# Optimization experiments

Hardware: AMD Instinct MI355X
Metric: run time of the kernel (lower is better)

## Reference

```python
import jax, jax.numpy as jnp
import numpy as np

N, M = 120000, 32
VX, VY = 0.16, 0.16
X_OFF = VX / 2 + 0.0          # vx/2 + pc_range[0]
Y_OFF = VY / 2 + (-39.68)     # vy/2 + pc_range[1]
BN_EPS = 1e-3


def setup_inputs() -> dict:
    key = jax.random.key(0)
    k1, k2, k3, k4, k5 = jax.random.split(key, 5)
    features = jax.random.normal(k1, (N, M, 4), dtype=jnp.float32)
    num_points = jax.random.randint(k2, (N,), 1, M + 1)              # >=1 point per pillar
    cy = jax.random.randint(k3, (N, 1), 0, 496)
    cx = jax.random.randint(k4, (N, 1), 0, 432)
    zeros = jnp.zeros((N, 2), dtype=jnp.int32)
    coors = jnp.concatenate([zeros, cy, cx], axis=1)                 # (N,4): [b, z, y, x]
    W = jax.random.normal(k5, (63, 9), dtype=jnp.float32) * 0.1      # Linear(9->63), no bias
    gamma = jnp.ones((63,), jnp.float32)
    beta = jnp.zeros((63,), jnp.float32)
    running_mean = jnp.zeros((63,), jnp.float32)
    running_var = jnp.ones((63,), jnp.float32)
    return {"features": features, "num_points": num_points, "coors": coors,
            "W": W, "gamma": gamma, "beta": beta,
            "running_mean": running_mean, "running_var": running_var}


def reference(features, num_points, coors, W, gamma, beta, running_mean, running_var):
    dt = features.dtype
    npf = num_points.astype(dt)[:, None, None]                        # (N,1,1)
    # distance to pillar centroid (xyz mean over points)
    voxels_mean = features[:, :, :3].sum(axis=1, keepdims=True) / npf
    centroid_dist = features[:, :, :3] - voxels_mean                  # (N,M,3)
    # offset from pillar base center (detached in the original)
    fxy = jax.lax.stop_gradient(features[:, :, :2])
    cx = fxy[:, :, 0] - (coors[:, 3].astype(dt)[:, None] * VX + X_OFF)
    cy = fxy[:, :, 1] - (coors[:, 2].astype(dt)[:, None] * VY + Y_OFF)
    base_center = jnp.stack([cx, cy], axis=-1)                        # (N,M,2)
    feats = jnp.concatenate([features, centroid_dist, base_center], axis=-1)  # (N,M,9)
    # zero out padded points
    mask = (jnp.arange(feats.shape[1])[None, :] < num_points[:, None]).astype(dt)[:, :, None]
    feats = feats * mask
    # PFNLayer (last layer, mode='max'): linear -> BN (eval stats) -> relu -> max over points
    x = jnp.einsum('nmc,uc->nmu', feats, W)                           # (N,M,63)
    inv = gamma / jnp.sqrt(running_var + BN_EPS)
    x = x * inv + (beta - running_mean * inv)
    x = jax.nn.relu(x)
    x_max = x.max(axis=1)                                             # (N,63)
    return jnp.concatenate([x_max, num_points.astype(dt)[:, None]], axis=-1)  # (N,64)
```

## Files before the change

### kernel.cpp

```cpp
#include <hip/hip_runtime.h>
#include <hip/hip_bf16.h>

typedef unsigned int u32;
typedef __attribute__((ext_vector_type(8))) short bf16x8;
typedef __attribute__((ext_vector_type(16))) float f32x16;
typedef __attribute__((ext_vector_type(4))) u32 u32x4;


#define XOFF (0.08f)
#define YOFF (0.08f - 39.68f)

__device__ __forceinline__ u32 f2bf_bits(float f) {
    union { float f; u32 u; } v; v.f = f;
    u32 u = v.u;
    u += 0x7fffu + ((u >> 16) & 1u);
    return u >> 16;
}
__device__ __forceinline__ short bf1(float f) { return (short)f2bf_bits(f); }

__device__ __forceinline__ u32 pk2(float lo, float hi) {
    __hip_bfloat162 h = __float22bfloat162_rn(make_float2(lo, hi));
    union { __hip_bfloat162 h; u32 u; } v; v.h = h;
    return v.u;
}

__device__ __forceinline__ float vmax16(const f32x16 v) {
    float m = fmaxf(fmaxf(v[0], v[1]), v[2]);
    m = fmaxf(fmaxf(m, v[3]), v[4]);
    m = fmaxf(fmaxf(m, v[5]), v[6]);
    m = fmaxf(fmaxf(m, v[7]), v[8]);
    m = fmaxf(fmaxf(m, v[9]), v[10]);
    m = fmaxf(fmaxf(m, v[11]), v[12]);
    m = fmaxf(fmaxf(m, v[13]), v[14]);
    return fmaxf(m, v[15]);
}

__global__ __launch_bounds__(256, 4)
void pfn_mfma(const float* __restrict__ features,
              const int* __restrict__ num_points,
              const int* __restrict__ coors,
              const float* __restrict__ W,
              const float* __restrict__ gamma,
              const float* __restrict__ beta,
              const float* __restrict__ rmean,
              const float* __restrict__ rvar,
              float* __restrict__ out,
              int n_total)
{
    const int lane = threadIdx.x & 63;
    const int wid  = threadIdx.x >> 6;
    const int half = lane >> 5;
    const int m    = lane & 31;
    const int waves_total = gridDim.x * 4;
    const int gwave = blockIdx.x * 4 + wid;

    const int c0 = m, c1 = 32 + m;
    const float inv0   = gamma[c0] / sqrtf(rvar[c0] + 1e-3f);
    const float shift0 = beta[c0] - rmean[c0] * inv0;
    float inv1 = 0.0f, shift1 = 0.0f;
    if (c1 < 63) {
        inv1   = gamma[c1] / sqrtf(rvar[c1] + 1e-3f);
        shift1 = beta[c1] - rmean[c1] * inv1;
    }

    bf16x8 b0, b1;
#pragma unroll
    for (int j = 0; j < 8; ++j) {
        const int k = half * 8 + j;
        float w0v = 0.0f, w1v = 0.0f;
        if (k < 9)       { w0v = W[c0 * 9 + k] * inv0;
                           w1v = (c1 < 63) ? W[c1 * 9 + k] * inv1 : 0.0f; }
        else if (k == 9) { w0v = shift0; w1v = shift1; }
        b0[j] = bf1(w0v);
        b1[j] = bf1(w1v);
    }

    const f32x16 zacc = {};
    const float4* featv = reinterpret_cast<const float4*>(features);
    const int n_pairs = (n_total + 1) >> 1;
    const int iters = (n_pairs + waves_total - 1) / waves_total;

    int pair = gwave;
    int nh   = min(min(pair, n_pairs - 1) * 2 + half, n_total - 1);
    int npts = num_points[nh];
    int2 cc  = *reinterpret_cast<const int2*>(coors + nh * 4 + 2);
    float4 q = featv[nh * 32 + m];

    for (int it = 0; it < iters; ++it) {
        const int pn  = pair + waves_total;
        const int nhn = min(min(pn, n_pairs - 1) * 2 + half, n_total - 1);
        const int npn = num_points[nhn];
        const int2 ccn = *reinterpret_cast<const int2*>(coors + nhn * 4 + 2);
        const float4 qn = featv[nhn * 32 + m];

        float sx = q.x, sy = q.y, sz = q.z;
#pragma unroll
        for (int d = 1; d < 32; d <<= 1) {
            sx += __shfl_xor(sx, d, 32);
            sy += __shfl_xor(sy, d, 32);
            sz += __shfl_xor(sz, d, 32);
        }
        const float rnp = __builtin_amdgcn_rcpf((float)npts);
        const float mx = sx * rnp, my = sy * rnp, mz = sz * rnp;
        const float cxo = (float)cc.y * 0.16f + XOFF;
        const float cyo = (float)cc.x * 0.16f + YOFF;

        u32 p0 = pk2(q.x, q.y);
        u32 p1 = pk2(q.z, q.w);
        u32 p2 = pk2(q.x - mx, q.y - my);
        u32 p3 = pk2(q.z - mz, q.x - cxo);
        if (m >= npts) { p0 = 0; p1 = 0; p2 = 0; p3 = 0; }
        const u32 p4 = pk2((m < npts) ? q.y - cyo : 0.0f, 1.0f);

        const u32 x0 = __shfl_xor(p0, 32);
        const u32 x1 = __shfl_xor(p1, 32);
        const u32 x2 = __shfl_xor(p2, 32);
        const u32 x3 = __shfl_xor(p3, 32);
        const u32 x4 = __shfl_xor(p4, 32);

        u32x4 adw, bdw;
        adw[0] = half ? x4 : p0;  adw[1] = half ? 0u : p1;
        adw[2] = half ? 0u : p2;  adw[3] = half ? 0u : p3;
        bdw[0] = half ? p4 : x0;  bdw[1] = half ? 0u : x1;
        bdw[2] = half ? 0u : x2;  bdw[3] = half ? 0u : x3;
        const bf16x8 aA = __builtin_bit_cast(bf16x8, adw);
        const bf16x8 aB = __builtin_bit_cast(bf16x8, bdw);

        const f32x16 cA0 = __builtin_amdgcn_mfma_f32_32x32x16_bf16(aA, b0, zacc, 0, 0, 0);
        const f32x16 cA1 = __builtin_amdgcn_mfma_f32_32x32x16_bf16(aA, b1, zacc, 0, 0, 0);
        float tA0 = vmax16(cA0);
        float tA1 = vmax16(cA1);
        const f32x16 cB0 = __builtin_amdgcn_mfma_f32_32x32x16_bf16(aB, b0, zacc, 0, 0, 0);
        const f32x16 cB1 = __builtin_amdgcn_mfma_f32_32x32x16_bf16(aB, b1, zacc, 0, 0, 0);
        float tB0 = vmax16(cB0);
        float tB1 = vmax16(cB1);

        tA0 = fmaxf(tA0, __shfl_xor(tA0, 32));
        tA1 = fmaxf(tA1, __shfl_xor(tA1, 32));
        tB0 = fmaxf(tB0, __shfl_xor(tB0, 32));
        tB1 = fmaxf(tB1, __shfl_xor(tB1, 32));

        float vA = fmaxf(half ? tA1 : tA0, 0.0f);
        float vB = fmaxf(half ? tB1 : tB0, 0.0f);

        const float npf = (float)npts;
        const float npA = __shfl(npf, 0);
        const float npB = __shfl(npf, 32);
        if (lane == 63) { vA = npA; vB = npB; }

        if (pair < n_pairs) {
            const int nA = pair * 2;
            out[nA * 64 + lane] = vA;
            if (nA + 1 < n_total) out[(nA + 1) * 64 + lane] = vB;
        }

        pair = pn; q = qn; npts = npn; cc = ccn;
    }
}

extern "C" void kernel_launch(void* const* d_in, const int* in_sizes, int n_in,
                              void* d_out, int out_size, void* d_ws, size_t ws_size,
                              hipStream_t stream) {
    const float* features   = (const float*)d_in[0];
    const int*   num_points = (const int*)d_in[1];
    const int*   coors      = (const int*)d_in[2];
    const float* W          = (const float*)d_in[3];
    const float* gamma      = (const float*)d_in[4];
    const float* beta       = (const float*)d_in[5];
    const float* rmean      = (const float*)d_in[6];
    const float* rvar       = (const float*)d_in[7];
    float* out              = (float*)d_out;

    const int n_total = in_sizes[1];

    const int blocks = 2048;
    pfn_mfma<<<blocks, 256, 0, stream>>>(features, num_points, coors, W,
                                         gamma, beta, rmean, rvar, out, n_total);
}
```

Before: 125.2 us.

## Process two pillar pairs per iteration with ds_swizzle reductions and deeper prefetch

```diff
diff --git a/kernel.cpp b/kernel.cpp
--- a/kernel.cpp
+++ b/kernel.cpp
@@ -9,6 +9,10 @@
 
 #define XOFF (0.08f)
 #define YOFF (0.08f - 39.68f)
+
+#define SWZ_ADD(s, imm)                                                        \
+    s += __builtin_bit_cast(float, __builtin_amdgcn_ds_swizzle(                \
+             __builtin_bit_cast(int, s), imm))
 
 __device__ __forceinline__ u32 f2bf_bits(float f) {
     union { float f; u32 u; } v; v.f = f;
@@ -33,6 +37,77 @@
     m = fmaxf(fmaxf(m, v[11]), v[12]);
     m = fmaxf(fmaxf(m, v[13]), v[14]);
     return fmaxf(m, v[15]);
+}
+
+__device__ __forceinline__ void frontend(const float4 q, const int npts,
+                                         const int2 cc, const int m,
+                                         const int half,
+                                         bf16x8& aA, bf16x8& aB)
+{
+    float sx = q.x, sy = q.y, sz = q.z;
+    SWZ_ADD(sx, 0x041F); SWZ_ADD(sy, 0x041F); SWZ_ADD(sz, 0x041F);
+    SWZ_ADD(sx, 0x081F); SWZ_ADD(sy, 0x081F); SWZ_ADD(sz, 0x081F);
+    SWZ_ADD(sx, 0x101F); SWZ_ADD(sy, 0x101F); SWZ_ADD(sz, 0x101F);
+    SWZ_ADD(sx, 0x201F); SWZ_ADD(sy, 0x201F); SWZ_ADD(sz, 0x201F);
+    SWZ_ADD(sx, 0x401F); SWZ_ADD(sy, 0x401F); SWZ_ADD(sz, 0x401F);
+
+    const float rnp = __builtin_amdgcn_rcpf((float)npts);
+    const float mx = sx * rnp, my = sy * rnp, mz = sz * rnp;
+    const float cxo = (float)cc.y * 0.16f + XOFF;
+    const float cyo = (float)cc.x * 0.16f + YOFF;
+
+    u32 p0 = pk2(q.x, q.y);
+    u32 p1 = pk2(q.z, q.w);
+    u32 p2 = pk2(q.x - mx, q.y - my);
+    u32 p3 = pk2(q.z - mz, q.x - cxo);
+    if (m >= npts) { p0 = 0; p1 = 0; p2 = 0; p3 = 0; }
+    const u32 p4 = pk2((m < npts) ? q.y - cyo : 0.0f, 1.0f);
+
+    const u32 x0 = __shfl_xor(p0, 32);
+    const u32 x1 = __shfl_xor(p1, 32);
+    const u32 x2 = __shfl_xor(p2, 32);
+    const u32 x3 = __shfl_xor(p3, 32);
+    const u32 x4 = __shfl_xor(p4, 32);
+
+    u32x4 adw, bdw;
+    adw[0] = half ? x4 : p0;  adw[1] = half ? 0u : p1;
+    adw[2] = half ? 0u : p2;  adw[3] = half ? 0u : p3;
+    bdw[0] = half ? p4 : x0;  bdw[1] = half ? 0u : x1;
+    bdw[2] = half ? 0u : x2;  bdw[3] = half ? 0u : x3;
+    aA = __builtin_bit_cast(bf16x8, adw);
+    aB = __builtin_bit_cast(bf16x8, bdw);
+}
+
+__device__ __forceinline__ void backend(const bf16x8 aA, const bf16x8 aB,
+                                        const bf16x8 b0, const bf16x8 b1,
+                                        const f32x16 zacc, const int half,
+                                        const int lane, const float npf,
+                                        const int pairIdx, const int n_pairs,
+                                        const int n_total,
+                                        float* __restrict__ out)
+{
+    const f32x16 cA0 = __builtin_amdgcn_mfma_f32_32x32x16_bf16(aA, b0, zacc, 0, 0, 0);
+    const f32x16 cA1 = __builtin_amdgcn_mfma_f32_32x32x16_bf16(aA, b1, zacc, 0, 0, 0);
+    const float tA0 = vmax16(cA0);
+    const float tA1 = vmax16(cA1);
+    const f32x16 cB0 = __builtin_amdgcn_mfma_f32_32x32x16_bf16(aB, b0, zacc, 0, 0, 0);
+    const f32x16 cB1 = __builtin_amdgcn_mfma_f32_32x32x16_bf16(aB, b1, zacc, 0, 0, 0);
+    const float tB0 = vmax16(cB0);
+    const float tB1 = vmax16(cB1);
+
+    const float keepA = half ? tA1 : tA0, sendA = half ? tA0 : tA1;
+    const float keepB = half ? tB1 : tB0, sendB = half ? tB0 : tB1;
+    float vA = fmaxf(fmaxf(keepA, __shfl_xor(sendA, 32)), 0.0f);
+    float vB = fmaxf(fmaxf(keepB, __shfl_xor(sendB, 32)), 0.0f);
+
+    const float npo = __shfl_xor(npf, 32);
+    if (lane == 63) { vA = npo; vB = npf; }
+
+    if (pairIdx < n_pairs) {
+        const int nA = pairIdx * 2;
+        out[nA * 64 + lane] = vA;
+        if (nA + 1 < n_total) out[(nA + 1) * 64 + lane] = vB;
+    }
 }
 
 __global__ __launch_bounds__(256, 4)
@@ -78,83 +153,39 @@
     const f32x16 zacc = {};
     const float4* featv = reinterpret_cast<const float4*>(features);
     const int n_pairs = (n_total + 1) >> 1;
-    const int iters = (n_pairs + waves_total - 1) / waves_total;
-
-    int pair = gwave;
-    int nh   = min(min(pair, n_pairs - 1) * 2 + half, n_total - 1);
-    int npts = num_points[nh];
-    int2 cc  = *reinterpret_cast<const int2*>(coors + nh * 4 + 2);
-    float4 q = featv[nh * 32 + m];
+    const int stride  = waves_total * 2;
+    const int iters   = (n_pairs + stride - 1) / stride;
+
+    auto load_pair = [&](int pr, float4& q, int& np, int2& cc) {
+        int nh = min(pr, n_pairs - 1) * 2 + half;
+        nh = min(nh, n_total - 1);
+        np = num_points[nh];
+        cc = *reinterpret_cast<const int2*>(coors + nh * 4 + 2);
+        q  = featv[nh * 32 + m];
+    };
+
+    int pa = gwave;
+    float4 qa, qb; int na_, nb_; int2 ca, cb;
+    load_pair(pa, qa, na_, ca);
+    load_pair(pa + waves_total, qb, nb_, cb);
 
     for (int it = 0; it < iters; ++it) {
-        const int pn  = pair + waves_total;
-        const int nhn = min(min(pn, n_pairs - 1) * 2 + half, n_total - 1);
-        const int npn = num_points[nhn];
-        const int2 ccn = *reinterpret_cast<const int2*>(coors + nhn * 4 + 2);
-        const float4 qn = featv[nhn * 32 + m];
-
-        float sx = q.x, sy = q.y, sz = q.z;
-#pragma unroll
-        for (int d = 1; d < 32; d <<= 1) {
-            sx += __shfl_xor(sx, d, 32);
-            sy += __shfl_xor(sy, d, 32);
-            sz += __shfl_xor(sz, d, 32);
-        }
-        const float rnp = __builtin_amdgcn_rcpf((float)npts);
-        const float mx = sx * rnp, my = sy * rnp, mz = sz * rnp;
-        const float cxo = (float)cc.y * 0.16f + XOFF;
-        const float cyo = (float)cc.x * 0.16f + YOFF;
-
-        u32 p0 = pk2(q.x, q.y);
-        u32 p1 = pk2(q.z, q.w);
-        u32 p2 = pk2(q.x - mx, q.y - my);
-        u32 p3 = pk2(q.z - mz, q.x - cxo);
-        if (m >= npts) { p0 = 0; p1 = 0; p2 = 0; p3 = 0; }
-        const u32 p4 = pk2((m < npts) ? q.y - cyo : 0.0f, 1.0f);
-
-        const u32 x0 = __shfl_xor(p0, 32);
-        const u32 x1 = __shfl_xor(p1, 32);
-        const u32 x2 = __shfl_xor(p2, 32);
-        const u32 x3 = __shfl_xor(p3, 32);
-        const u32 x4 = __shfl_xor(p4, 32);
-
-        u32x4 adw, bdw;
-        adw[0] = half ? x4 : p0;  adw[1] = half ? 0u : p1;
-        adw[2] = half ? 0u : p2;  adw[3] = half ? 0u : p3;
-        bdw[0] = half ? p4 : x0;  bdw[1] = half ? 0u : x1;
-        bdw[2] = half ? 0u : x2;  bdw[3] = half ? 0u : x3;
-        const bf16x8 aA = __builtin_bit_cast(bf16x8, adw);
-        const bf16x8 aB = __builtin_bit_cast(bf16x8, bdw);
-
-        const f32x16 cA0 = __builtin_amdgcn_mfma_f32_32x32x16_bf16(aA, b0, zacc, 0, 0, 0);
-        const f32x16 cA1 = __builtin_amdgcn_mfma_f32_32x32x16_bf16(aA, b1, zacc, 0, 0, 0);
-        float tA0 = vmax16(cA0);
-        float tA1 = vmax16(cA1);
-        const f32x16 cB0 = __builtin_amdgcn_mfma_f32_32x32x16_bf16(aB, b0, zacc, 0, 0, 0);
-        const f32x16 cB1 = __builtin_amdgcn_mfma_f32_32x32x16_bf16(aB, b1, zacc, 0, 0, 0);
-        float tB0 = vmax16(cB0);
-        float tB1 = vmax16(cB1);
-
-        tA0 = fmaxf(tA0, __shfl_xor(tA0, 32));
-        tA1 = fmaxf(tA1, __shfl_xor(tA1, 32));
-        tB0 = fmaxf(tB0, __shfl_xor(tB0, 32));
-        tB1 = fmaxf(tB1, __shfl_xor(tB1, 32));
-
-        float vA = fmaxf(half ? tA1 : tA0, 0.0f);
-        float vB = fmaxf(half ? tB1 : tB0, 0.0f);
-
-        const float npf = (float)npts;
-        const float npA = __shfl(npf, 0);
-        const float npB = __shfl(npf, 32);
-        if (lane == 63) { vA = npA; vB = npB; }
-
-        if (pair < n_pairs) {
-            const int nA = pair * 2;
-            out[nA * 64 + lane] = vA;
-            if (nA + 1 < n_total) out[(nA + 1) * 64 + lane] = vB;
-        }
-
-        pair = pn; q = qn; npts = npn; cc = ccn;
+        float4 qan, qbn; int nan_, nbn_; int2 can, cbn;
+        load_pair(pa + stride, qan, nan_, can);
+        load_pair(pa + stride + waves_total, qbn, nbn_, cbn);
+
+        bf16x8 aA1, aB1, aA2, aB2;
+        frontend(qa, na_, ca, m, half, aA1, aB1);
+        frontend(qb, nb_, cb, m, half, aA2, aB2);
+
+        backend(aA1, aB1, b0, b1, zacc, half, lane, (float)na_,
+                pa,               n_pairs, n_total, out);
+        backend(aA2, aB2, b0, b1, zacc, half, lane, (float)nb_,
+                pa + waves_total, n_pairs, n_total, out);
+
+        pa += stride;
+        qa = qan; na_ = nan_; ca = can;
+        qb = qbn; nb_ = nbn_; cb = cbn;
     }
 }
 
```

New measurement: 125.0 us. About the same (-0.1%).

## Fold centroid and offset terms into the weights and compute sums with MFMA

Applied to the files above, without the earlier changes.

```diff
diff --git a/kernel.cpp b/kernel.cpp
--- a/kernel.cpp
+++ b/kernel.cpp
@@ -33,6 +33,27 @@
     m = fmaxf(fmaxf(m, v[11]), v[12]);
     m = fmaxf(fmaxf(m, v[13]), v[14]);
     return fmaxf(m, v[15]);
+}
+
+__device__ __forceinline__ float vsum16(const f32x16 v) {
+    const float a = (v[0] + v[1]) + (v[2] + v[3]);
+    const float b = (v[4] + v[5]) + (v[6] + v[7]);
+    const float c = (v[8] + v[9]) + (v[10] + v[11]);
+    const float d = (v[12] + v[13]) + (v[14] + v[15]);
+    return (a + b) + (c + d);
+}
+
+__device__ __forceinline__ float bc0(float v) {
+    return __builtin_bit_cast(float,
+        __builtin_amdgcn_ds_swizzle(__builtin_bit_cast(int, v), 0x0000));
+}
+__device__ __forceinline__ float bc1(float v) {
+    return __builtin_bit_cast(float,
+        __builtin_amdgcn_ds_swizzle(__builtin_bit_cast(int, v), 0x0020));
+}
+__device__ __forceinline__ float bc2(float v) {
+    return __builtin_bit_cast(float,
+        __builtin_amdgcn_ds_swizzle(__builtin_bit_cast(int, v), 0x0040));
 }
 
 __global__ __launch_bounds__(256, 4)
@@ -62,99 +83,132 @@
         inv1   = gamma[c1] / sqrtf(rvar[c1] + 1e-3f);
         shift1 = beta[c1] - rmean[c1] * inv1;
     }
-
-    bf16x8 b0, b1;
+    const float shift_me = half ? shift1 : shift0;
+
+    float wp0[9], wp1[9];
+#pragma unroll
+    for (int c = 0; c < 9; ++c) {
+        wp0[c] = W[c0 * 9 + c] * inv0;
+        wp1[c] = (c1 < 63) ? W[c1 * 9 + c] * inv1 : 0.0f;
+    }
+    auto rowv = [](int k, const float* wp, float sh) -> float {
+        switch (k) {
+            case 0:  return wp[0] + wp[4] + wp[7];
+            case 1:  return wp[1] + wp[5] + wp[8];
+            case 2:  return wp[2] + wp[6];
+            case 3:  return wp[3];
+            case 4:  return -30000.0f;
+            case 5:  return sh;
+            case 6:  return wp[4];
+            case 7:  return wp[5];
+            case 8:  return wp[6];
+            case 9:  return wp[7];
+            case 10: return wp[8];
+            default: return 0.0f;
+        }
+    };
+    bf16x8 b0, b1, bs;
 #pragma unroll
     for (int j = 0; j < 8; ++j) {
         const int k = half * 8 + j;
-        float w0v = 0.0f, w1v = 0.0f;
-        if (k < 9)       { w0v = W[c0 * 9 + k] * inv0;
-                           w1v = (c1 < 63) ? W[c1 * 9 + k] * inv1 : 0.0f; }
-        else if (k == 9) { w0v = shift0; w1v = shift1; }
-        b0[j] = bf1(w0v);
-        b1[j] = bf1(w1v);
+        b0[j] = bf1(rowv(k, wp0, shift0));
+        b1[j] = bf1(rowv(k, wp1, shift1));
+        bs[j] = (half == 0 && j == m && m < 3) ? bf1(1.0f) : (short)0;
     }
 
     const f32x16 zacc = {};
     const float4* featv = reinterpret_cast<const float4*>(features);
     const int n_pairs = (n_total + 1) >> 1;
-    const int iters = (n_pairs + waves_total - 1) / waves_total;
-
-    int pair = gwave;
-    int nh   = min(min(pair, n_pairs - 1) * 2 + half, n_total - 1);
-    int npts = num_points[nh];
-    int2 cc  = *reinterpret_cast<const int2*>(coors + nh * 4 + 2);
-    float4 q = featv[nh * 32 + m];
+    const int iters   = (n_pairs + waves_total - 1) / waves_total;
+
+    struct PairIn { float4 q; int npA, npB; int2 ccA, ccB; };
+    auto load_pair = [&](int pr) -> PairIn {
+        PairIn r;
+        const int base = min(pr, n_pairs - 1) * 2;
+        const int iB   = min(base + 1, n_total - 1);
+        const int nh   = min(base + half, n_total - 1);
+        r.npA = num_points[base];
+        r.npB = num_points[iB];
+        r.ccA = *reinterpret_cast<const int2*>(coors + base * 4 + 2);
+        r.ccB = *reinterpret_cast<const int2*>(coors + iB * 4 + 2);
+        r.q   = featv[nh * 32 + m];
+        return r;
+    };
+
+    int pa = gwave;
+    PairIn cur = load_pair(pa);
 
     for (int it = 0; it < iters; ++it) {
-        const int pn  = pair + waves_total;
-        const int nhn = min(min(pn, n_pairs - 1) * 2 + half, n_total - 1);
-        const int npn = num_points[nhn];
-        const int2 ccn = *reinterpret_cast<const int2*>(coors + nhn * 4 + 2);
-        const float4 qn = featv[nhn * 32 + m];
-
-        float sx = q.x, sy = q.y, sz = q.z;
-#pragma unroll
-        for (int d = 1; d < 32; d <<= 1) {
-            sx += __shfl_xor(sx, d, 32);
-            sy += __shfl_xor(sy, d, 32);
-            sz += __shfl_xor(sz, d, 32);
-        }
-        const float rnp = __builtin_amdgcn_rcpf((float)npts);
-        const float mx = sx * rnp, my = sy * rnp, mz = sz * rnp;
-        const float cxo = (float)cc.y * 0.16f + XOFF;
-        const float cyo = (float)cc.x * 0.16f + YOFF;
-
-        u32 p0 = pk2(q.x, q.y);
-        u32 p1 = pk2(q.z, q.w);
-        u32 p2 = pk2(q.x - mx, q.y - my);
-        u32 p3 = pk2(q.z - mz, q.x - cxo);
-        if (m >= npts) { p0 = 0; p1 = 0; p2 = 0; p3 = 0; }
-        const u32 p4 = pk2((m < npts) ? q.y - cyo : 0.0f, 1.0f);
-
+        PairIn nx = load_pair(pa + waves_total);
+
+        const float4 q = cur.q;
+        const u32 p0 = pk2(q.x, q.y);
+        const u32 p1 = pk2(q.z, q.w);
         const u32 x0 = __shfl_xor(p0, 32);
         const u32 x1 = __shfl_xor(p1, 32);
-        const u32 x2 = __shfl_xor(p2, 32);
-        const u32 x3 = __shfl_xor(p3, 32);
-        const u32 x4 = __shfl_xor(p4, 32);
-
-        u32x4 adw, bdw;
-        adw[0] = half ? x4 : p0;  adw[1] = half ? 0u : p1;
-        adw[2] = half ? 0u : p2;  adw[3] = half ? 0u : p3;
-        bdw[0] = half ? p4 : x0;  bdw[1] = half ? 0u : x1;
-        bdw[2] = half ? 0u : x2;  bdw[3] = half ? 0u : x3;
-        const bf16x8 aA = __builtin_bit_cast(bf16x8, adw);
-        const bf16x8 aB = __builtin_bit_cast(bf16x8, bdw);
+
+        u32x4 sa4 = {half ? 0u : p0, half ? 0u : p1, 0u, 0u};
+        u32x4 sb4 = {half ? 0u : x0, half ? 0u : x1, 0u, 0u};
+        const f32x16 sA = __builtin_amdgcn_mfma_f32_32x32x16_bf16(
+            __builtin_bit_cast(bf16x8, sa4), bs, zacc, 0, 0, 0);
+        const f32x16 sB = __builtin_amdgcn_mfma_f32_32x32x16_bf16(
+            __builtin_bit_cast(bf16x8, sb4), bs, zacc, 0, 0, 0);
+        float tA = vsum16(sA); tA += __shfl_xor(tA, 32);
+        float tB = vsum16(sB); tB += __shfl_xor(tB, 32);
+        const float sxA = bc0(tA), syA = bc1(tA), szA = bc2(tA);
+        const float sxB = bc0(tB), syB = bc1(tB), szB = bc2(tB);
+
+        const float rnpA = __builtin_amdgcn_rcpf((float)cur.npA);
+        const float rnpB = __builtin_amdgcn_rcpf((float)cur.npB);
+        const float cxoA = (float)cur.ccA.y * 0.16f + XOFF;
+        const float cyoA = (float)cur.ccA.x * 0.16f + YOFF;
+        const float cxoB = (float)cur.ccB.y * 0.16f + XOFF;
+        const float cyoB = (float)cur.ccB.x * 0.16f + YOFF;
+        const u32 d2A = pk2((m < cur.npA) ? 0.0f : 1.0f, 1.0f);
+        const u32 d2B = pk2((m < cur.npB) ? 0.0f : 1.0f, 1.0f);
+        const u32 d3A = pk2(-sxA * rnpA, -syA * rnpA);
+        const u32 d3B = pk2(-sxB * rnpB, -syB * rnpB);
+        const u32 d4A = pk2(-szA * rnpA, -cxoA);
+        const u32 d4B = pk2(-szB * rnpB, -cxoB);
+        const u32 d5A = pk2(-cyoA, 0.0f);
+        const u32 d5B = pk2(-cyoB, 0.0f);
+
+        u32x4 aa = {half ? d4A : p0, half ? d5A : p1,
+                    half ? 0u : d2A, half ? 0u : d3A};
+        u32x4 ab = {half ? d4B : x0, half ? d5B : x1,
+                    half ? 0u : d2B, half ? 0u : d3B};
+        const bf16x8 aA = __builtin_bit_cast(bf16x8, aa);
+        const bf16x8 aB = __builtin_bit_cast(bf16x8, ab);
 
         const f32x16 cA0 = __builtin_amdgcn_mfma_f32_32x32x16_bf16(aA, b0, zacc, 0, 0, 0);
         const f32x16 cA1 = __builtin_amdgcn_mfma_f32_32x32x16_bf16(aA, b1, zacc, 0, 0, 0);
-        float tA0 = vmax16(cA0);
-        float tA1 = vmax16(cA1);
+        const float tA0 = vmax16(cA0);
+        const float tA1 = vmax16(cA1);
         const f32x16 cB0 = __builtin_amdgcn_mfma_f32_32x32x16_bf16(aB, b0, zacc, 0, 0, 0);
         const f32x16 cB1 = __builtin_amdgcn_mfma_f32_32x32x16_bf16(aB, b1, zacc, 0, 0, 0);
-        float tB0 = vmax16(cB0);
-        float tB1 = vmax16(cB1);
-
-        tA0 = fmaxf(tA0, __shfl_xor(tA0, 32));
-        tA1 = fmaxf(tA1, __shfl_xor(tA1, 32));
-        tB0 = fmaxf(tB0, __shfl_xor(tB0, 32));
-        tB1 = fmaxf(tB1, __shfl_xor(tB1, 32));
-
-        float vA = fmaxf(half ? tA1 : tA0, 0.0f);
-        float vB = fmaxf(half ? tB1 : tB0, 0.0f);
-
-        const float npf = (float)npts;
-        const float npA = __shfl(npf, 0);
-        const float npB = __shfl(npf, 32);
-        if (lane == 63) { vA = npA; vB = npB; }
-
-        if (pair < n_pairs) {
-            const int nA = pair * 2;
+        const float tB0 = vmax16(cB0);
+        const float tB1 = vmax16(cB1);
+
+        const float keepA = half ? tA1 : tA0, sendA = half ? tA0 : tA1;
+        const float keepB = half ? tB1 : tB0, sendB = half ? tB0 : tB1;
+        float vA = fmaxf(keepA, __shfl_xor(sendA, 32));
+        float vB = fmaxf(keepB, __shfl_xor(sendB, 32));
+
+        if (cur.npA < 32) vA = fmaxf(vA, shift_me);
+        if (cur.npB < 32) vB = fmaxf(vB, shift_me);
+        vA = fmaxf(vA, 0.0f);
+        vB = fmaxf(vB, 0.0f);
+
+        if (lane == 63) { vA = (float)cur.npA; vB = (float)cur.npB; }
+
+        if (pa < n_pairs) {
+            const int nA = pa * 2;
             out[nA * 64 + lane] = vA;
             if (nA + 1 < n_total) out[(nA + 1) * 64 + lane] = vB;
         }
 
-        pair = pn; q = qn; npts = npn; cc = ccn;
+        pa += waves_total;
+        cur = nx;
     }
 }
 
```

New measurement: 132.6 us. 5.9% more time.
